# Kernel optimization log

Hardware: AMD Instinct MI355X
Metric: run time of the kernel (lower is better)

## Reference

```python
import jax, jax.numpy as jnp
import numpy as np
from jax import lax

B, M = 16384, 200            # flattened batch*time, tokens per observation
NUM_LAYERS, OW, OH = 22, 11, 11
HIDDEN = 512

_MAX_VEC = jnp.maximum(jnp.array([9.0, 1.0, 1.0, 10.0, 3.0, 254.0, 1.0, 1.0, 235.0, 8.0,
                                  9.0, 250.0, 29.0, 1.0, 1.0, 8.0, 1.0, 1.0, 6.0, 3.0,
                                  1.0, 2.0], dtype=jnp.float32), 1.0)


def setup_inputs() -> dict:
    key = jax.random.key(0)
    ks = jax.random.split(key, 10)
    init = lambda k, shp, std: (jax.random.normal(k, shp, dtype=jnp.float32) * std)
    observations = jax.random.randint(ks[0], (B, M, 3), 0, 255, dtype=jnp.int32)
    return {
        "observations": observations,
        # CNN: Conv2d(22,128,5,s=3) -> Conv2d(128,128,3,s=1) -> Linear(128,256)
        "conv1_w": init(ks[1], (128, NUM_LAYERS, 5, 5), 0.04), "conv1_b": jnp.zeros((128,), jnp.float32),
        "conv2_w": init(ks[2], (128, 128, 3, 3), 0.03),        "conv2_b": jnp.zeros((128,), jnp.float32),
        "fc_w": init(ks[3], (256, 128), 0.08),                 "fc_b": jnp.zeros((256,), jnp.float32),
        # self encoder Linear(22,256)
        "self_w": init(ks[4], (256, NUM_LAYERS), 0.2),         "self_b": jnp.zeros((256,), jnp.float32),
        # actor heads (nvec=[9,10]) and value head
        "actor0_w": init(ks[5], (9, HIDDEN), 0.01),            "actor0_b": jnp.zeros((9,), jnp.float32),
        "actor1_w": init(ks[6], (10, HIDDEN), 0.01),           "actor1_b": jnp.zeros((10,), jnp.float32),
        "value_w": init(ks[7], (1, HIDDEN), 1.0 / np.sqrt(HIDDEN)), "value_b": jnp.zeros((1,), jnp.float32),
    }


def reference(observations, conv1_w, conv1_b, conv2_w, conv2_b, fc_w, fc_b,
              self_w, self_b, actor0_w, actor0_b, actor1_w, actor1_b, value_w, value_b):
    # --- token parsing + scatter into dense grid ---
    obs = jnp.where(observations == 255, 0, observations)          # [B, M, 3]
    coords = obs[..., 0]
    x = (coords >> 4) & 15
    y = coords & 15
    atr = obs[..., 1]
    vals = obs[..., 2].astype(jnp.float32)
    valid = (coords != 255) & (x < OW) & (y < OH) & (atr < NUM_LAYERS)
    atr_s = jnp.where(valid, atr, NUM_LAYERS)                      # route invalid OOB -> dropped
    b_idx = jnp.broadcast_to(jnp.arange(B)[:, None], atr.shape)
    box = jnp.zeros((B, NUM_LAYERS, OW, OH), jnp.float32)
    box = box.at[b_idx, atr_s, x, y].set(vals, mode='drop')
    feat = box / (_MAX_VEC[None, :, None, None] + 1e-8)            # [B, 22, 11, 11]

    # --- self encoder on center cell ---
    self_f = jax.nn.relu(feat[:, :, 5, 5] @ self_w.T + self_b)     # [B, 256]

    # --- CNN trunk ---
    h = lax.conv_general_dilated(feat, conv1_w, (3, 3), 'VALID')   # [B, 128, 3, 3]
    h = jax.nn.relu(h + conv1_b[None, :, None, None])
    h = lax.conv_general_dilated(h, conv2_w, (1, 1), 'VALID')      # [B, 128, 1, 1]
    h = jax.nn.relu(h + conv2_b[None, :, None, None]).reshape(B, -1)
    cnn_f = jax.nn.relu(h @ fc_w.T + fc_b)                         # [B, 256]

    hidden = jnp.concatenate([self_f, cnn_f], axis=1)              # [B, 512]

    # --- heads ---
    a0 = hidden @ actor0_w.T + actor0_b                            # [B, 9]
    a1 = hidden @ actor1_w.T + actor1_b                            # [B, 10]
    v = hidden @ value_w.T + value_b                               # [B, 1]
    return a0, a1, v
```

## Files before the change

kernel.cpp:

```cpp
#include <hip/hip_runtime.h>
#include <stdint.h>

typedef __bf16 bf16x8 __attribute__((ext_vector_type(8)));
typedef float  f32x4  __attribute__((ext_vector_type(4)));

#define B_TOT 16384
#define GS    4
#define MB2   32
#define NPREP 1076

#define OFF_W1T   0u
#define OFF_W2B   141312u
#define OFF_FCB   436224u
#define OFF_WH    501760u
#define OFF_BH    534528u
#define OFF_SWB   534656u
#define OFF_SELFV 551040u
#define OFF_PCG   1599616u
#define OFF_ENT   2189440u

__device__ const float d_maxv[22] = {
  9.f,1.f,1.f,10.f,3.f,254.f,1.f,1.f,235.f,8.f,
  9.f,250.f,29.f,1.f,1.f,8.f,1.f,1.f,6.f,3.f,1.f,2.f };

static __device__ __forceinline__ short f2bf(float f){
  union { float f; uint32_t u; } c; c.f = f;
  uint32_t r = (c.u + 0x7FFFu + ((c.u >> 16) & 1u)) >> 16;
  return (short)r;
}
static __device__ __forceinline__ float bf2f(short s){
  union { uint32_t u; float f; } c; c.u = ((uint32_t)(uint16_t)s) << 16;
  return c.f;
}
static __device__ __forceinline__ uint32_t cvtpk(float lo, float hi){
  uint32_t pk;
  asm("v_cvt_pk_bf16_f32 %0, %1, %2" : "=v"(pk) : "v"(lo), "v"(hi));
  return pk;
}
static __device__ __forceinline__ int swz(int row, int k, int stride){
  return row * stride + ((((k >> 3) ^ (row & 7)) << 3) | (k & 7));
}
static __device__ __forceinline__ void gld16(const void* g, void* l){
  __builtin_amdgcn_global_load_lds(
      (const __attribute__((address_space(1))) void*)g,
      (__attribute__((address_space(3))) void*)l, 16, 0, 0);
}
static __device__ __forceinline__ void wavesync(){
  asm volatile("s_waitcnt lgkmcnt(0)" ::: "memory");
  __builtin_amdgcn_wave_barrier();
}

__global__ __launch_bounds__(256) void k_pt(
    const float* __restrict__ c1w, const float* __restrict__ c2w,
    const float* __restrict__ fcw, const float* __restrict__ a0w,
    const float* __restrict__ a1w, const float* __restrict__ vw,
    const float* __restrict__ a0b, const float* __restrict__ a1b,
    const float* __restrict__ vb,  const float* __restrict__ selfw,
    const int* __restrict__ obs,
    short* __restrict__ w1t, short* __restrict__ w2b, short* __restrict__ fcb,
    short* __restrict__ wh, float* __restrict__ bh, short* __restrict__ swB,
    short* __restrict__ selfvB, uint32_t* __restrict__ entG,
    uint32_t* __restrict__ pcntG)
{
  __shared__ uint32_t nzl[GS * 64];
  __shared__ uint32_t bkt[GS * 108];
  __shared__ uint32_t cnt[GS];
  __shared__ uint32_t pcnt[GS * 9];
  __shared__ float selfv[GS * 24];
  __shared__ float invS[22];

  if (blockIdx.x < NPREP) {
    int i = blockIdx.x * 256 + threadIdx.x;
    if (i < 70400) {
      int r = i >> 7, oc = i & 127;
      w1t[i] = f2bf(c1w[oc * 550 + r]);
    }
    i -= 70400;
    if (i >= 0 && i < 147456) {
      int oc = i / 1152, k = i - oc * 1152;
      int pos = k >> 7, ic = k & 127;
      w2b[i] = f2bf(c2w[oc * 1152 + ic * 9 + pos]);
    }
    i -= 147456;
    if (i >= 0 && i < 32768) fcb[i] = f2bf(fcw[i]);
    i -= 32768;
    if (i >= 0 && i < 16384) {
      int j = i >> 9, k = i & 511;
      float v = 0.f;
      if (j < 9) v = a0w[j * 512 + k];
      else if (j < 19) v = a1w[(j - 9) * 512 + k];
      else if (j == 19) v = vw[k];
      wh[i] = f2bf(v);
    }
    i -= 16384;
    if (i >= 0 && i < 32) {
      float v = 0.f;
      if (i < 9) v = a0b[i]; else if (i < 19) v = a1b[i - 9]; else if (i == 19) v = vb[0];
      bh[i] = v;
    }
    i -= 32;
    if (i >= 0 && i < 8192) {
      int o = i >> 5, l = i & 31;
      swB[i] = (l < 22) ? f2bf(selfw[o * 22 + l]) : (short)0;
    }
    return;
  }

  const int tid = threadIdx.x, wid = tid >> 6, lane = tid & 63;
  const int b = (blockIdx.x - NPREP) * GS + wid;

  if (lane == 0) cnt[wid] = 0u;
  if (lane < 9)  pcnt[wid * 9 + lane] = 0u;
  if (lane < 24) selfv[wid * 24 + lane] = 0.f;
  for (int i = lane; i < 108; i += 64) bkt[wid * 108 + i] = 0u;
  if (tid < 22) invS[tid] = 1.0f / (d_maxv[tid] + 1e-8f);
  __syncthreads();

  {
    const int* base = obs + (size_t)b * 600;
    #pragma unroll
    for (int k = 0; k < 4; ++k) {
      int m = lane + (k << 6);
      if (m < 200) {
        int c = base[m * 3], a = base[m * 3 + 1], v = base[m * 3 + 2];
        c = (c == 255) ? 0 : c;  a = (a == 255) ? 0 : a;  v = (v == 255) ? 0 : v;
        int x = (c >> 4) & 15, y = c & 15;
        if (x < 11 && y < 11 && a < 22) {
          uint32_t cell = (uint32_t)(a * 121 + x * 11 + y);
          uint32_t idx = atomicAdd(&cnt[wid], 1u);
          if (idx < 64u)
            nzl[wid * 64 + idx] = ((uint32_t)m << 20) | (cell << 8) | (uint32_t)v;
        }
      }
    }
  }
  wavesync();

  {
    uint32_t n = cnt[wid]; if (n > 64u) n = 64u;
    for (uint32_t i = lane; i < n; i += 64) {
      uint32_t e = nzl[wid * 64 + i];
      uint32_t cell = (e >> 8) & 0xFFFu;
      uint32_t best = e;
      for (uint32_t j = 0; j < n; ++j) {
        uint32_t ej = nzl[wid * 64 + j];
        if ((((ej >> 8) & 0xFFFu) == cell) && ej > best) best = ej;
      }
      if (best == e && (e & 255u) != 0u) {
        uint32_t v8 = e & 255u;
        uint32_t l = cell / 121u, rem = cell - l * 121u;
        uint32_t x = rem / 11u, y = rem - x * 11u;
        if (rem == 60u)
          selfv[wid * 24 + l] = (float)v8 * invS[l];
        #pragma unroll
        for (int ox = 0; ox < 3; ++ox) {
          int kx = (int)x - 3 * ox; if (kx < 0 || kx > 4) continue;
          #pragma unroll
          for (int oy = 0; oy < 3; ++oy) {
            int ky = (int)y - 3 * oy; if (ky < 0 || ky > 4) continue;
            uint32_t r = l * 25u + (uint32_t)kx * 5u + (uint32_t)ky;
            uint32_t p = (uint32_t)(ox * 3 + oy);
            uint32_t s = atomicAdd(&pcnt[wid * 9 + p], 1u);
            if (s < 12u)
              bkt[wid * 108 + p * 12 + s] = (r << 13) | (l << 8) | v8;
          }
        }
      }
    }
  }
  wavesync();

  if (lane < 16) {
    int l0 = lane * 2;
    float v0 = (l0     < 22) ? selfv[wid * 24 + l0]     : 0.f;
    float v1 = (l0 + 1 < 22) ? selfv[wid * 24 + l0 + 1] : 0.f;
    *(uint32_t*)(selfvB + (size_t)b * 32 + l0) = cvtpk(v0, v1);
  }
  for (int i = lane; i < 108; i += 64) entG[(size_t)b * 108 + i] = bkt[wid * 108 + i];
  if (lane < 9) {
    uint32_t m = pcnt[wid * 9 + lane];
    pcntG[(size_t)b * 9 + lane] = (m > 12u) ? 12u : m;
  }
}

__global__ __launch_bounds__(512, 4) void k_mlp(
    const uint32_t* __restrict__ entG, const uint32_t* __restrict__ pcntG,
    const short* __restrict__ selfvB, const short* __restrict__ w1t,
    const short* __restrict__ w2b, const short* __restrict__ fcb,
    const short* __restrict__ wh,  const short* __restrict__ swB,
    const float* __restrict__ c1b, const float* __restrict__ c2b,
    const float* __restrict__ fcbias, const float* __restrict__ selfb,
    const float* __restrict__ bh, float* __restrict__ out)
{
  __shared__ __align__(16) short smem[28032];
  uint32_t* tokS  = (uint32_t*)(smem + 20480);
  uint32_t* pcntS = (uint32_t*)(smem + 27392);
  float*    invL  = (float*)(smem + 27968);
  short*    Atile = smem + 16384;

  const int tid  = threadIdx.x, wid = tid >> 6, lane = tid & 63;
  const int l15 = lane & 15, kg = lane >> 4;
  const int wr = wid & 1, wc = wid >> 1;
  const int rowA = wr * 16 + l15;
  const size_t b0 = (size_t)blockIdx.x * MB2;
  const f32x4 z4 = {0.f, 0.f, 0.f, 0.f};

  const int cb1 = tid >> 4;
  const int icg = tid & 15;
  const int ic0 = icg * 8;

  {
    const int4* src = (const int4*)(entG + b0 * 108);
    int4* dst = (int4*)tokS;
    for (int i = tid; i < 864; i += 512) dst[i] = src[i];
  }
  if (tid < 288) pcntS[tid] = pcntG[b0 * 9 + tid];
  if (tid < 22) invL[tid] = 1.0f / (d_maxv[tid] + 1e-8f);

  float bz[8];
  #pragma unroll
  for (int j = 0; j < 8; ++j) bz[j] = c1b[ic0 + j];

  const int sub = lane >> 3, pch = lane & 7;
  const int ocj0 = (wid * 2) * 8 + sub, ocj1 = (wid * 2 + 1) * 8 + sub;
  const short* gB0 = w2b + (size_t)ocj0 * 1152 + ((pch ^ (ocj0 & 7)) << 3);
  const short* gB1 = w2b + (size_t)ocj1 * 1152 + ((pch ^ (ocj1 & 7)) << 3);
  const int dB0 = (wid * 2) * 512, dB1 = (wid * 2 + 1) * 512;

  gld16(gB0, &smem[dB0]); gld16(gB1, &smem[dB1]);
  __syncthreads();

  f32x4 acc[2] = {z4, z4};
  for (int t = 0; t < 18; ++t) {
    if ((t & 1) == 0) {
      const int p = t >> 1;
      float a8[8];
      #pragma unroll
      for (int j = 0; j < 8; ++j) a8[j] = bz[j];
      const int n = (int)pcntS[cb1 * 9 + p];
      for (int i = 0; i < n; ++i) {
        uint32_t e = tokS[cb1 * 108 + p * 12 + i];
        int r = (int)(e >> 13);
        float vf = (float)(e & 255u) * invL[(e >> 8) & 31u];
        const uint32_t* wp = (const uint32_t*)(const void*)&w1t[r * 128 + ic0];
        uint32_t w0 = wp[0], w1 = wp[1], w2 = wp[2], w3 = wp[3];
        a8[0] += vf * bf2f((short)(w0 & 0xFFFFu));
        a8[1] += vf * bf2f((short)(w0 >> 16));
        a8[2] += vf * bf2f((short)(w1 & 0xFFFFu));
        a8[3] += vf * bf2f((short)(w1 >> 16));
        a8[4] += vf * bf2f((short)(w2 & 0xFFFFu));
        a8[5] += vf * bf2f((short)(w2 >> 16));
        a8[6] += vf * bf2f((short)(w3 & 0xFFFFu));
        a8[7] += vf * bf2f((short)(w3 >> 16));
      }
      uint32_t* ad = (uint32_t*)(void*)&Atile[swz(cb1, ic0, 128)];
      ad[0] = cvtpk(fmaxf(a8[0], 0.f), fmaxf(a8[1], 0.f));
      ad[1] = cvtpk(fmaxf(a8[2], 0.f), fmaxf(a8[3], 0.f));
      ad[2] = cvtpk(fmaxf(a8[4], 0.f), fmaxf(a8[5], 0.f));
      ad[3] = cvtpk(fmaxf(a8[6], 0.f), fmaxf(a8[7], 0.f));
    }
    const int cbB = (t & 1) * 8192;
    if (t < 17) {
      const int nbB = 8192 - cbB;
      const int ko = (t + 1) * 64;
      gld16(gB0 + ko, &smem[nbB + dB0]);
      gld16(gB1 + ko, &smem[nbB + dB1]);
      asm volatile("s_waitcnt vmcnt(2) lgkmcnt(0)" ::: "memory");
    } else {
      asm volatile("s_waitcnt vmcnt(0) lgkmcnt(0)" ::: "memory");
    }
    __builtin_amdgcn_sched_barrier(0);
    __builtin_amdgcn_s_barrier();
    __builtin_amdgcn_sched_barrier(0);
    #pragma unroll
    for (int ks = 0; ks < 2; ++ks) {
      int kq = ks * 4 + kg;
      int icA = (t & 1) * 64 + kq * 8;
      bf16x8 a = *(const bf16x8*)(const void*)&Atile[swz(rowA, icA, 128)];
      #pragma unroll
      for (int nf = 0; nf < 2; ++nf) {
        int oc = wc * 32 + nf * 16 + l15;
        bf16x8 bv = *(const bf16x8*)(const void*)
                    &smem[cbB + oc * 64 + ((kq ^ (oc & 7)) << 3)];
        acc[nf] = __builtin_amdgcn_mfma_f32_16x16x32_bf16(a, bv, acc[nf], 0, 0, 0);
      }
    }
    __builtin_amdgcn_sched_barrier(0);
    __builtin_amdgcn_s_barrier();
  }
  #pragma unroll
  for (int nf = 0; nf < 2; ++nf) {
    int col = wc * 32 + nf * 16 + l15;
    float bias = c2b[col];
    #pragma unroll
    for (int rr = 0; rr < 4; ++rr) {
      int row = wr * 16 + kg * 4 + rr;
      smem[swz(row, col, 128)] = f2bf(fmaxf(acc[nf][rr] + bias, 0.f));
    }
  }
  __syncthreads();

  {
    f32x4 fca[4] = {z4, z4, z4, z4};
    #pragma unroll
    for (int kk = 0; kk < 4; ++kk) {
      int k = kk * 32 + kg * 8;
      bf16x8 a = *(const bf16x8*)(const void*)&smem[swz(rowA, k, 128)];
      #pragma unroll
      for (int nf = 0; nf < 4; ++nf) {
        int col = wc * 64 + nf * 16 + l15;
        bf16x8 bv = *(const bf16x8*)(const void*)(fcb + (size_t)col * 128 + k);
        fca[nf] = __builtin_amdgcn_mfma_f32_16x16x32_bf16(a, bv, fca[nf], 0, 0, 0);
      }
    }
    #pragma unroll
    for (int nf = 0; nf < 4; ++nf) {
      int col = wc * 64 + nf * 16 + l15;
      float bias = fcbias[col];
      #pragma unroll
      for (int rr = 0; rr < 4; ++rr) {
        int row = wr * 16 + kg * 4 + rr;
        smem[4096 + swz(row, col, 256)] = f2bf(fmaxf(fca[nf][rr] + bias, 0.f));
      }
    }
  }
  {
    f32x4 sa[4] = {z4, z4, z4, z4};
    bf16x8 a = *(const bf16x8*)(const void*)
               (selfvB + (b0 + (size_t)rowA) * 32 + kg * 8);
    #pragma unroll
    for (int nf = 0; nf < 4; ++nf) {
      int col = wc * 64 + nf * 16 + l15;
      bf16x8 bv = *(const bf16x8*)(const void*)(swB + (size_t)col * 32 + kg * 8);
      sa[nf] = __builtin_amdgcn_mfma_f32_16x16x32_bf16(a, bv, sa[nf], 0, 0, 0);
    }
    #pragma unroll
    for (int nf = 0; nf < 4; ++nf) {
      int col = wc * 64 + nf * 16 + l15;
      float bias = selfb[col];
      #pragma unroll
      for (int rr = 0; rr < 4; ++rr) {
        int row = wr * 16 + kg * 4 + rr;
        smem[12288 + swz(row, col, 256)] = f2bf(fmaxf(sa[nf][rr] + bias, 0.f));
      }
    }
  }
  __syncthreads();

  {
    float* hacc = (float*)smem;
    const int kh = (wid >> 1) & 1, nh = wid >> 2;
    const int ncol = nh * 16 + l15;
    f32x4 ha = z4;
    #pragma unroll
    for (int kk = 0; kk < 8; ++kk) {
      int kl = kk * 32 + kg * 8;
      bf16x8 a;
      if (kh == 0) a = *(const bf16x8*)(const void*)&smem[12288 + swz(rowA, kl, 256)];
      else         a = *(const bf16x8*)(const void*)&smem[4096  + swz(rowA, kl, 256)];
      bf16x8 bv = *(const bf16x8*)(const void*)(wh + (size_t)ncol * 512 + kh * 256 + kl);
      ha = __builtin_amdgcn_mfma_f32_16x16x32_bf16(a, bv, ha, 0, 0, 0);
    }
    #pragma unroll
    for (int rr = 0; rr < 4; ++rr) {
      int row = wr * 16 + kg * 4 + rr;
      hacc[kh * 1024 + row * 32 + ncol] = ha[rr];
    }
  }
  __syncthreads();

  {
    const float* hacc = (const float*)smem;
    #pragma unroll
    for (int q = 0; q < 2; ++q) {
      int i = q * 512 + tid;
      int row = i >> 5, colh = i & 31;
      float v = hacc[i] + hacc[1024 + i] + bh[colh];
      int gr = (int)b0 + row;
      if (colh < 9)        out[gr * 9 + colh] = v;
      else if (colh < 19)  out[147456 + gr * 10 + (colh - 9)] = v;
      else if (colh == 19) out[311296 + gr] = v;
    }
  }
}

extern "C" void kernel_launch(void* const* d_in, const int* in_sizes, int n_in,
                              void* d_out, int out_size, void* d_ws, size_t ws_size,
                              hipStream_t stream)
{
  const int*   obs = (const int*)  d_in[0];
  const float* c1w = (const float*)d_in[1];
  const float* c1b = (const float*)d_in[2];
  const float* c2w = (const float*)d_in[3];
  const float* c2b = (const float*)d_in[4];
  const float* fcw = (const float*)d_in[5];
  const float* fcbv= (const float*)d_in[6];
  const float* sw  = (const float*)d_in[7];
  const float* sb  = (const float*)d_in[8];
  const float* a0w = (const float*)d_in[9];
  const float* a0b = (const float*)d_in[10];
  const float* a1w = (const float*)d_in[11];
  const float* a1b = (const float*)d_in[12];
  const float* vw  = (const float*)d_in[13];
  const float* vb  = (const float*)d_in[14];

  char* ws = (char*)d_ws;
  short* w1t    = (short*)(ws + OFF_W1T);
  short* w2b    = (short*)(ws + OFF_W2B);
  short* fcb    = (short*)(ws + OFF_FCB);
  short* wh     = (short*)(ws + OFF_WH);
  float* bh     = (float*)(ws + OFF_BH);
  short* swB    = (short*)(ws + OFF_SWB);
  short* selfvB = (short*)(ws + OFF_SELFV);
  uint32_t* pcG = (uint32_t*)(ws + OFF_PCG);
  uint32_t* enG = (uint32_t*)(ws + OFF_ENT);
  float* out    = (float*)d_out;

  k_pt<<<dim3(NPREP + B_TOT / GS), dim3(256), 0, stream>>>(
      c1w, c2w, fcw, a0w, a1w, vw, a0b, a1b, vb, sw, obs,
      w1t, w2b, fcb, wh, bh, swB, selfvB, enG, pcG);
  k_mlp<<<dim3(B_TOT / MB2), dim3(512), 0, stream>>>(enG, pcG, selfvB, w1t, w2b,
                                                     fcb, wh, swB, c1b, c2b,
                                                     fcbv, sb, bh, out);
}
```

Before: 54.23 us.

## Halve MLP block rows and compute full conv1 tile before conv2 pipeline

The MLP kernel now handles 16 batch rows per block instead of 32, which doubles the grid. Conv1 outputs for all 9 positions are computed up front into a large shared-memory A tile, with each thread producing 4 channels. This takes the conv1 work out of the conv2 K-loop, so that loop only streams conv2 weight chunks and issues one MFMA per k-step per wave. The head reduction is split four ways over K. Each block now reloads the conv2/fc weights for half as many rows, and shared memory use grows to about 77KB, which may limit occupancy.

```diff
diff --git a/kernel.cpp b/kernel.cpp
--- a/kernel.cpp
+++ b/kernel.cpp
@@ -6,7 +6,7 @@
 
 #define B_TOT 16384
 #define GS    4
-#define MB2   32
+#define MB2   16
 #define NPREP 1076
 
 #define OFF_W1T   0u
@@ -192,82 +192,73 @@
     const float* __restrict__ fcbias, const float* __restrict__ selfb,
     const float* __restrict__ bh, float* __restrict__ out)
 {
-  __shared__ __align__(16) short smem[28032];
-  uint32_t* tokS  = (uint32_t*)(smem + 20480);
-  uint32_t* pcntS = (uint32_t*)(smem + 27392);
-  float*    invL  = (float*)(smem + 27968);
-  short*    Atile = smem + 16384;
+  __shared__ __align__(16) short smem[38604];
+  uint32_t* tokS  = (uint32_t*)(smem + 34816);
+  uint32_t* pcntS = (uint32_t*)(smem + 38272);
+  float*    invL  = (float*)(smem + 38560);
+  short*    Bb    = smem + 18432;
 
   const int tid  = threadIdx.x, wid = tid >> 6, lane = tid & 63;
   const int l15 = lane & 15, kg = lane >> 4;
-  const int wr = wid & 1, wc = wid >> 1;
-  const int rowA = wr * 16 + l15;
+  const int wc = wid;
   const size_t b0 = (size_t)blockIdx.x * MB2;
   const f32x4 z4 = {0.f, 0.f, 0.f, 0.f};
 
-  const int cb1 = tid >> 4;
-  const int icg = tid & 15;
-  const int ic0 = icg * 8;
-
   {
     const int4* src = (const int4*)(entG + b0 * 108);
     int4* dst = (int4*)tokS;
-    for (int i = tid; i < 864; i += 512) dst[i] = src[i];
-  }
-  if (tid < 288) pcntS[tid] = pcntG[b0 * 9 + tid];
+    for (int i = tid; i < 432; i += 512) dst[i] = src[i];
+  }
+  if (tid < 144) pcntS[tid] = pcntG[b0 * 9 + tid];
   if (tid < 22) invL[tid] = 1.0f / (d_maxv[tid] + 1e-8f);
-
-  float bz[8];
-  #pragma unroll
-  for (int j = 0; j < 8; ++j) bz[j] = c1b[ic0 + j];
 
   const int sub = lane >> 3, pch = lane & 7;
   const int ocj0 = (wid * 2) * 8 + sub, ocj1 = (wid * 2 + 1) * 8 + sub;
   const short* gB0 = w2b + (size_t)ocj0 * 1152 + ((pch ^ (ocj0 & 7)) << 3);
   const short* gB1 = w2b + (size_t)ocj1 * 1152 + ((pch ^ (ocj1 & 7)) << 3);
   const int dB0 = (wid * 2) * 512, dB1 = (wid * 2 + 1) * 512;
-
-  gld16(gB0, &smem[dB0]); gld16(gB1, &smem[dB1]);
-  __syncthreads();
-
-  f32x4 acc[2] = {z4, z4};
-  for (int t = 0; t < 18; ++t) {
-    if ((t & 1) == 0) {
-      const int p = t >> 1;
-      float a8[8];
-      #pragma unroll
-      for (int j = 0; j < 8; ++j) a8[j] = bz[j];
+  gld16(gB0, &Bb[dB0]); gld16(gB1, &Bb[dB1]);
+  __syncthreads();
+
+  {
+    const int cb1 = tid >> 5;
+    const int ic0 = (tid & 31) * 4;
+    float bzv[4];
+    #pragma unroll
+    for (int j = 0; j < 4; ++j) bzv[j] = c1b[ic0 + j];
+    #pragma unroll
+    for (int p = 0; p < 9; ++p) {
+      float a4[4] = {bzv[0], bzv[1], bzv[2], bzv[3]};
       const int n = (int)pcntS[cb1 * 9 + p];
       for (int i = 0; i < n; ++i) {
         uint32_t e = tokS[cb1 * 108 + p * 12 + i];
         int r = (int)(e >> 13);
         float vf = (float)(e & 255u) * invL[(e >> 8) & 31u];
         const uint32_t* wp = (const uint32_t*)(const void*)&w1t[r * 128 + ic0];
-        uint32_t w0 = wp[0], w1 = wp[1], w2 = wp[2], w3 = wp[3];
-        a8[0] += vf * bf2f((short)(w0 & 0xFFFFu));
-        a8[1] += vf * bf2f((short)(w0 >> 16));
-        a8[2] += vf * bf2f((short)(w1 & 0xFFFFu));
-        a8[3] += vf * bf2f((short)(w1 >> 16));
-        a8[4] += vf * bf2f((short)(w2 & 0xFFFFu));
-        a8[5] += vf * bf2f((short)(w2 >> 16));
-        a8[6] += vf * bf2f((short)(w3 & 0xFFFFu));
-        a8[7] += vf * bf2f((short)(w3 >> 16));
-      }
-      uint32_t* ad = (uint32_t*)(void*)&Atile[swz(cb1, ic0, 128)];
-      ad[0] = cvtpk(fmaxf(a8[0], 0.f), fmaxf(a8[1], 0.f));
-      ad[1] = cvtpk(fmaxf(a8[2], 0.f), fmaxf(a8[3], 0.f));
-      ad[2] = cvtpk(fmaxf(a8[4], 0.f), fmaxf(a8[5], 0.f));
-      ad[3] = cvtpk(fmaxf(a8[6], 0.f), fmaxf(a8[7], 0.f));
-    }
+        uint32_t w0 = wp[0], w1 = wp[1];
+        a4[0] += vf * bf2f((short)(w0 & 0xFFFFu));
+        a4[1] += vf * bf2f((short)(w0 >> 16));
+        a4[2] += vf * bf2f((short)(w1 & 0xFFFFu));
+        a4[3] += vf * bf2f((short)(w1 >> 16));
+      }
+      uint32_t* ad = (uint32_t*)(void*)&smem[swz(cb1, p * 128 + ic0, 1152)];
+      ad[0] = cvtpk(fmaxf(a4[0], 0.f), fmaxf(a4[1], 0.f));
+      ad[1] = cvtpk(fmaxf(a4[2], 0.f), fmaxf(a4[3], 0.f));
+    }
+  }
+  __syncthreads();
+
+  f32x4 acc = z4;
+  for (int t = 0; t < 18; ++t) {
     const int cbB = (t & 1) * 8192;
     if (t < 17) {
       const int nbB = 8192 - cbB;
       const int ko = (t + 1) * 64;
-      gld16(gB0 + ko, &smem[nbB + dB0]);
-      gld16(gB1 + ko, &smem[nbB + dB1]);
-      asm volatile("s_waitcnt vmcnt(2) lgkmcnt(0)" ::: "memory");
+      gld16(gB0 + ko, &Bb[nbB + dB0]);
+      gld16(gB1 + ko, &Bb[nbB + dB1]);
+      asm volatile("s_waitcnt vmcnt(2)" ::: "memory");
     } else {
-      asm volatile("s_waitcnt vmcnt(0) lgkmcnt(0)" ::: "memory");
+      asm volatile("s_waitcnt vmcnt(0)" ::: "memory");
     }
     __builtin_amdgcn_sched_barrier(0);
     __builtin_amdgcn_s_barrier();
@@ -275,112 +266,108 @@
     #pragma unroll
     for (int ks = 0; ks < 2; ++ks) {
       int kq = ks * 4 + kg;
-      int icA = (t & 1) * 64 + kq * 8;
-      bf16x8 a = *(const bf16x8*)(const void*)&Atile[swz(rowA, icA, 128)];
+      bf16x8 a = *(const bf16x8*)(const void*)
+                 &smem[swz(l15, t * 64 + kq * 8, 1152)];
+      int oc = wc * 16 + l15;
+      bf16x8 bv = *(const bf16x8*)(const void*)
+                  &Bb[cbB + oc * 64 + ((kq ^ (oc & 7)) << 3)];
+      acc = __builtin_amdgcn_mfma_f32_16x16x32_bf16(a, bv, acc, 0, 0, 0);
+    }
+    __builtin_amdgcn_sched_barrier(0);
+    __builtin_amdgcn_s_barrier();
+  }
+  __syncthreads();
+
+  {
+    int col = wc * 16 + l15;
+    float bias = c2b[col];
+    #pragma unroll
+    for (int rr = 0; rr < 4; ++rr) {
+      int row = kg * 4 + rr;
+      smem[swz(row, col, 128)] = f2bf(fmaxf(acc[rr] + bias, 0.f));
+    }
+  }
+  __syncthreads();
+
+  {
+    f32x4 fca[2] = {z4, z4};
+    #pragma unroll
+    for (int kk = 0; kk < 4; ++kk) {
+      int k = kk * 32 + kg * 8;
+      bf16x8 a = *(const bf16x8*)(const void*)&smem[swz(l15, k, 128)];
       #pragma unroll
       for (int nf = 0; nf < 2; ++nf) {
-        int oc = wc * 32 + nf * 16 + l15;
-        bf16x8 bv = *(const bf16x8*)(const void*)
-                    &smem[cbB + oc * 64 + ((kq ^ (oc & 7)) << 3)];
-        acc[nf] = __builtin_amdgcn_mfma_f32_16x16x32_bf16(a, bv, acc[nf], 0, 0, 0);
-      }
-    }
-    __builtin_amdgcn_sched_barrier(0);
-    __builtin_amdgcn_s_barrier();
-  }
-  #pragma unroll
-  for (int nf = 0; nf < 2; ++nf) {
-    int col = wc * 32 + nf * 16 + l15;
-    float bias = c2b[col];
-    #pragma unroll
-    for (int rr = 0; rr < 4; ++rr) {
-      int row = wr * 16 + kg * 4 + rr;
-      smem[swz(row, col, 128)] = f2bf(fmaxf(acc[nf][rr] + bias, 0.f));
-    }
-  }
-  __syncthreads();
-
-  {
-    f32x4 fca[4] = {z4, z4, z4, z4};
-    #pragma unroll
-    for (int kk = 0; kk < 4; ++kk) {
-      int k = kk * 32 + kg * 8;
-      bf16x8 a = *(const bf16x8*)(const void*)&smem[swz(rowA, k, 128)];
-      #pragma unroll
-      for (int nf = 0; nf < 4; ++nf) {
-        int col = wc * 64 + nf * 16 + l15;
+        int col = wc * 32 + nf * 16 + l15;
         bf16x8 bv = *(const bf16x8*)(const void*)(fcb + (size_t)col * 128 + k);
         fca[nf] = __builtin_amdgcn_mfma_f32_16x16x32_bf16(a, bv, fca[nf], 0, 0, 0);
       }
     }
     #pragma unroll
-    for (int nf = 0; nf < 4; ++nf) {
-      int col = wc * 64 + nf * 16 + l15;
+    for (int nf = 0; nf < 2; ++nf) {
+      int col = wc * 32 + nf * 16 + l15;
       float bias = fcbias[col];
       #pragma unroll
       for (int rr = 0; rr < 4; ++rr) {
-        int row = wr * 16 + kg * 4 + rr;
-        smem[4096 + swz(row, col, 256)] = f2bf(fmaxf(fca[nf][rr] + bias, 0.f));
-      }
-    }
-  }
-  {
-    f32x4 sa[4] = {z4, z4, z4, z4};
+        int row = kg * 4 + rr;
+        smem[2048 + swz(row, col, 256)] = f2bf(fmaxf(fca[nf][rr] + bias, 0.f));
+      }
+    }
+  }
+  {
+    f32x4 sa[2] = {z4, z4};
     bf16x8 a = *(const bf16x8*)(const void*)
-               (selfvB + (b0 + (size_t)rowA) * 32 + kg * 8);
-    #pragma unroll
-    for (int nf = 0; nf < 4; ++nf) {
-      int col = wc * 64 + nf * 16 + l15;
+               (selfvB + (b0 + (size_t)l15) * 32 + kg * 8);
+    #pragma unroll
+    for (int nf = 0; nf < 2; ++nf) {
+      int col = wc * 32 + nf * 16 + l15;
       bf16x8 bv = *(const bf16x8*)(const void*)(swB + (size_t)col * 32 + kg * 8);
       sa[nf] = __builtin_amdgcn_mfma_f32_16x16x32_bf16(a, bv, sa[nf], 0, 0, 0);
     }
     #pragma unroll
-    for (int nf = 0; nf < 4; ++nf) {
-      int col = wc * 64 + nf * 16 + l15;
+    for (int nf = 0; nf < 2; ++nf) {
+      int col = wc * 32 + nf * 16 + l15;
       float bias = selfb[col];
       #pragma unroll
       for (int rr = 0; rr < 4; ++rr) {
-        int row = wr * 16 + kg * 4 + rr;
-        smem[12288 + swz(row, col, 256)] = f2bf(fmaxf(sa[nf][rr] + bias, 0.f));
-      }
-    }
-  }
-  __syncthreads();
-
-  {
-    float* hacc = (float*)smem;
-    const int kh = (wid >> 1) & 1, nh = wid >> 2;
+        int row = kg * 4 + rr;
+        smem[6144 + swz(row, col, 256)] = f2bf(fmaxf(sa[nf][rr] + bias, 0.f));
+      }
+    }
+  }
+  __syncthreads();
+
+  {
+    float* hacc = (float*)(smem + 10240);
+    const int kq = wid & 3, nh = wid >> 2;
     const int ncol = nh * 16 + l15;
     f32x4 ha = z4;
     #pragma unroll
-    for (int kk = 0; kk < 8; ++kk) {
+    for (int kk = 0; kk < 4; ++kk) {
       int kl = kk * 32 + kg * 8;
+      int kglob = kq * 128 + kl;
       bf16x8 a;
-      if (kh == 0) a = *(const bf16x8*)(const void*)&smem[12288 + swz(rowA, kl, 256)];
-      else         a = *(const bf16x8*)(const void*)&smem[4096  + swz(rowA, kl, 256)];
-      bf16x8 bv = *(const bf16x8*)(const void*)(wh + (size_t)ncol * 512 + kh * 256 + kl);
+      if (kq < 2) a = *(const bf16x8*)(const void*)&smem[6144 + swz(l15, kglob, 256)];
+      else        a = *(const bf16x8*)(const void*)&smem[2048 + swz(l15, kglob - 256, 256)];
+      bf16x8 bv = *(const bf16x8*)(const void*)(wh + (size_t)ncol * 512 + kglob);
       ha = __builtin_amdgcn_mfma_f32_16x16x32_bf16(a, bv, ha, 0, 0, 0);
     }
     #pragma unroll
     for (int rr = 0; rr < 4; ++rr) {
-      int row = wr * 16 + kg * 4 + rr;
-      hacc[kh * 1024 + row * 32 + ncol] = ha[rr];
-    }
-  }
-  __syncthreads();
-
-  {
-    const float* hacc = (const float*)smem;
-    #pragma unroll
-    for (int q = 0; q < 2; ++q) {
-      int i = q * 512 + tid;
-      int row = i >> 5, colh = i & 31;
-      float v = hacc[i] + hacc[1024 + i] + bh[colh];
-      int gr = (int)b0 + row;
-      if (colh < 9)        out[gr * 9 + colh] = v;
-      else if (colh < 19)  out[147456 + gr * 10 + (colh - 9)] = v;
-      else if (colh == 19) out[311296 + gr] = v;
-    }
+      int row = kg * 4 + rr;
+      hacc[kq * 512 + row * 32 + ncol] = ha[rr];
+    }
+  }
+  __syncthreads();
+
+  {
+    const float* hacc = (const float*)(smem + 10240);
+    int row = tid >> 5, colh = tid & 31;
+    float v = hacc[tid] + hacc[512 + tid] + hacc[1024 + tid] + hacc[1536 + tid]
+            + bh[colh];
+    int gr = (int)b0 + row;
+    if (colh < 9)        out[gr * 9 + colh] = v;
+    else if (colh < 19)  out[147456 + gr * 10 + (colh - 9)] = v;
+    else if (colh == 19) out[311296 + gr] = v;
   }
 }
 
```

After: 60.57 us. 11.7% more time.
